# Kernel tuning notes

Hardware: AMD Instinct MI355X
Metric: run time of the kernel (lower is better)

Reference implementation:

```python
import jax, jax.numpy as jnp
import numpy as np

N_NODES = 100_000
N_EDGES = 3_200_000
NUM_FEATURES = 128
EMB = 128
GNN_LAYERS = 3
N_GRAPHS = 512
FILL = 2.0  # improved=True -> self-loop weight 2


def setup_inputs() -> dict:
    key = jax.random.key(0)
    ks = jax.random.split(key, 8)
    x = jax.random.normal(ks[0], (N_NODES, NUM_FEATURES), jnp.float32)
    edge_index = jax.random.randint(ks[1], (2, N_EDGES), 0, N_NODES, dtype=jnp.int64)
    batch_index = jnp.sort(jax.random.randint(ks[2], (N_NODES,), 0, N_GRAPHS, dtype=jnp.int64))
    W0 = jax.random.normal(ks[3], (NUM_FEATURES, EMB), jnp.float32) / np.float32(np.sqrt(NUM_FEATURES))
    b0 = jnp.zeros((EMB,), jnp.float32)
    W_hid = jax.random.normal(ks[4], (GNN_LAYERS - 1, EMB, EMB), jnp.float32) / np.float32(np.sqrt(EMB))
    b_hid = jnp.zeros((GNN_LAYERS - 1, EMB), jnp.float32)
    W_out = jax.random.normal(ks[5], (2 * EMB, 1), jnp.float32) / np.float32(np.sqrt(2 * EMB))
    b_out = jnp.zeros((1,), jnp.float32)
    return {"x": x, "edge_index": edge_index, "batch_index": batch_index,
            "W0": W0, "b0": b0, "W_hid": W_hid, "b_hid": b_hid,
            "W_out": W_out, "b_out": b_out}


def _gcn_norm(edge_index, n_nodes):
    # add self-loops (weight=FILL for improved=True), symmetric D^-1/2 A D^-1/2 norm
    loop = jnp.arange(n_nodes)
    row = jnp.concatenate([edge_index[0], loop])
    col = jnp.concatenate([edge_index[1], loop])
    w = jnp.concatenate([jnp.ones((edge_index.shape[1],), jnp.float32),
                         jnp.full((n_nodes,), FILL, jnp.float32)])
    deg = jax.ops.segment_sum(w, col, num_segments=n_nodes)
    dinv = jnp.where(deg > 0, jax.lax.rsqrt(deg), 0.0)
    return row, col, dinv[row] * w * dinv[col]


def _gcn_conv(h, W, b, row, col, norm, n_nodes):
    h = h @ W                              # [N, emb]
    msg = h[row] * norm[:, None]           # gather + scale over edges
    return jax.ops.segment_sum(msg, col, num_segments=n_nodes) + b


def reference(x, edge_index, batch_index, W0, b0, W_hid, b_hid, W_out, b_out):
    n = x.shape[0]
    row, col, norm = _gcn_norm(edge_index, n)
    h = jnp.tanh(_gcn_conv(x, W0, b0, row, col, norm, n))
    for i in range(W_hid.shape[0]):
        h = jnp.tanh(_gcn_conv(h, W_hid[i], b_hid[i], row, col, norm, n))
    cnt = jax.ops.segment_sum(jnp.ones((n,), h.dtype), batch_index, num_segments=N_GRAPHS)
    mx = jax.ops.segment_max(h, batch_index, num_segments=N_GRAPHS)
    mx = jnp.where(cnt[:, None] > 0, mx, 0.0)            # gmp
    mean = jax.ops.segment_sum(h, batch_index, num_segments=N_GRAPHS) / jnp.maximum(cnt, 1.0)[:, None]  # gap
    pooled = jnp.concatenate([mx, mean], axis=1)          # [G, 2*emb]
    return pooled @ W_out + b_out                         # [G, 1]
```

## Files before the change

### kernel.cpp

```cpp
#include <hip/hip_runtime.h>
#include <math.h>

#define NF 128
#define SCAN_CHUNK 1024
#define BUCK_SHIFT 9
#define BUCK_CAP 20480
#define NBUCK_MAX 256
#define ECHUNK 2048

typedef int      vint4   __attribute__((ext_vector_type(4)));
typedef float    vfloat4 __attribute__((ext_vector_type(4)));
typedef float    f32x4   __attribute__((ext_vector_type(4)));
typedef _Float16 vhalf4  __attribute__((ext_vector_type(4)));
typedef _Float16 vhalf8  __attribute__((ext_vector_type(8)));

__global__ __launch_bounds__(256) void k_bucket(const int* __restrict__ row,
                                                const int* __restrict__ col,
                                                int* __restrict__ gcur,
                                                int* __restrict__ bdata, int E) {
  __shared__ int bcnt[NBUCK_MAX];
  __shared__ int bstage[NBUCK_MAX][32];
  const int tid = threadIdx.x;
  const int nChunks = (E + ECHUNK - 1) / ECHUNK;

  for (int chunk = blockIdx.x; chunk < nChunks; chunk += gridDim.x) {
    bcnt[tid] = 0;
    __syncthreads();

    const int cbase = chunk * ECHUNK;
    if (cbase + ECHUNK <= E) {
      const vint4* r4 = reinterpret_cast<const vint4*>(row) + (cbase >> 2) + 2 * tid;
      const vint4* c4 = reinterpret_cast<const vint4*>(col) + (cbase >> 2) + 2 * tid;
      vint4 ra = __builtin_nontemporal_load(&r4[0]);
      vint4 rb = __builtin_nontemporal_load(&r4[1]);
      vint4 ca = __builtin_nontemporal_load(&c4[0]);
      vint4 cb = __builtin_nontemporal_load(&c4[1]);
      int rr[8] = {ra.x, ra.y, ra.z, ra.w, rb.x, rb.y, rb.z, rb.w};
      int cc[8] = {ca.x, ca.y, ca.z, ca.w, cb.x, cb.y, cb.z, cb.w};
#pragma unroll
      for (int j = 0; j < 8; ++j) {
        int b = cc[j] >> BUCK_SHIFT;
        int packed = ((cc[j] & ((1 << BUCK_SHIFT) - 1)) << 17) | rr[j];
        int pos = atomicAdd(&bcnt[b], 1);
        if (pos < 32) {
          bstage[b][pos] = packed;
        } else {
          int p = atomicAdd(&gcur[b], 1);
          if (p < BUCK_CAP) bdata[b * BUCK_CAP + p] = packed;
        }
      }
    } else {
      for (int j = 0; j < 8; ++j) {
        int e = cbase + tid + j * 256;
        if (e < E) {
          int c = col[e], r = row[e];
          int b = c >> BUCK_SHIFT;
          int packed = ((c & ((1 << BUCK_SHIFT) - 1)) << 17) | r;
          int pos = atomicAdd(&bcnt[b], 1);
          if (pos < 32) {
            bstage[b][pos] = packed;
          } else {
            int p = atomicAdd(&gcur[b], 1);
            if (p < BUCK_CAP) bdata[b * BUCK_CAP + p] = packed;
          }
        }
      }
    }
    __syncthreads();

    int k = bcnt[tid];
    if (k > 32) k = 32;
    if (k > 0) {
      int p = atomicAdd(&gcur[tid], k);
      for (int i = 0; i < k && p + i < BUCK_CAP; ++i)
        bdata[tid * BUCK_CAP + p + i] = bstage[tid][i];
    }
    __syncthreads();
  }
}

__global__ __launch_bounds__(256) void k_hist(const int* __restrict__ gcur,
                                              const int* __restrict__ bdata,
                                              int* __restrict__ cnt, int N) {
  __shared__ int hist[1 << BUCK_SHIFT];
  const int b = blockIdx.x;
  const int tid = threadIdx.x;
  hist[tid] = 0;
  hist[tid + 256] = 0;
  __syncthreads();
  int nb = gcur[b];
  if (nb > BUCK_CAP) nb = BUCK_CAP;
  const int* bd = bdata + (size_t)b * BUCK_CAP;
  for (int i = tid; i < nb; i += 256) atomicAdd(&hist[bd[i] >> 17], 1);
  __syncthreads();
  int base = b << BUCK_SHIFT;
#pragma unroll
  for (int k = 0; k < (1 << BUCK_SHIFT); k += 256) {
    int node = base + k + tid;
    if (node < N) cnt[node] = hist[k + tid];
  }
}

__global__ __launch_bounds__(256) void k_scanA(const int* __restrict__ cnt,
                                               int* __restrict__ chunkTot, int N) {
  int c0 = blockIdx.x * SCAN_CHUNK + threadIdx.x * 4;
  int s = 0;
#pragma unroll
  for (int j = 0; j < 4; ++j) {
    int idx = c0 + j;
    if (idx < N) s += cnt[idx];
  }
  __shared__ int red[256];
  red[threadIdx.x] = s;
  __syncthreads();
  for (int o = 128; o > 0; o >>= 1) {
    if (threadIdx.x < o) red[threadIdx.x] += red[threadIdx.x + o];
    __syncthreads();
  }
  if (threadIdx.x == 0) chunkTot[blockIdx.x] = red[0];
}

__global__ __launch_bounds__(128) void k_scanB(const int* __restrict__ chunkTot,
                                               int* __restrict__ chunkOff, int nChunks) {
  __shared__ int buf[128];
  int t = threadIdx.x;
  int v = (t < nChunks) ? chunkTot[t] : 0;
  buf[t] = v;
  __syncthreads();
  for (int o = 1; o < 128; o <<= 1) {
    int x = buf[t];
    if (t >= o) x += buf[t - o];
    __syncthreads();
    buf[t] = x;
    __syncthreads();
  }
  if (t < nChunks) chunkOff[t] = buf[t] - v;
}

__global__ __launch_bounds__(256) void k_scanC(const int* __restrict__ cnt,
                                               const int* __restrict__ chunkOff,
                                               int* __restrict__ offs,
                                               float* __restrict__ dinv, int N) {
  int t = threadIdx.x;
  int c0 = blockIdx.x * SCAN_CHUNK + t * 4;
  int v[4];
  int s = 0;
#pragma unroll
  for (int j = 0; j < 4; ++j) {
    int idx = c0 + j;
    v[j] = (idx < N) ? cnt[idx] : 0;
    s += v[j];
  }
  __shared__ int buf[256];
  buf[t] = s;
  __syncthreads();
  for (int o = 1; o < 256; o <<= 1) {
    int x = buf[t];
    if (t >= o) x += buf[t - o];
    __syncthreads();
    buf[t] = x;
    __syncthreads();
  }
  int excl = buf[t] - s + chunkOff[blockIdx.x];
#pragma unroll
  for (int j = 0; j < 4; ++j) {
    int idx = c0 + j;
    if (idx < N) {
      offs[idx] = excl;
      dinv[idx] = rsqrtf((float)v[j] + 2.0f);
      excl += v[j];
    }
  }
}

__global__ __launch_bounds__(256) void k_bfill(const int* __restrict__ gcur,
                                               const int* __restrict__ bdata,
                                               const int* __restrict__ offs,
                                               int* __restrict__ csr, int N) {
  __shared__ int lcur[1 << BUCK_SHIFT];
  const int b = blockIdx.x;
  const int tid = threadIdx.x;
  const int base = b << BUCK_SHIFT;
#pragma unroll
  for (int k = 0; k < (1 << BUCK_SHIFT); k += 256) {
    int node = base + k + tid;
    lcur[k + tid] = (node < N) ? offs[node] : 0;
  }
  __syncthreads();
  int nb = gcur[b];
  if (nb > BUCK_CAP) nb = BUCK_CAP;
  const int* bd = bdata + (size_t)b * BUCK_CAP;
  for (int i = tid; i < nb; i += 256) {
    int v = bd[i];
    int p = atomicAdd(&lcur[v >> 17], 1);
    csr[p] = v & 0x1FFFF;
  }
}

__global__ __launch_bounds__(256) void k_wcvt(const float* __restrict__ W0,
                                              const float* __restrict__ Whid,
                                              _Float16* __restrict__ wt) {
  int g = blockIdx.x * 1024 + threadIdx.x * 4;
#pragma unroll
  for (int j = 0; j < 4; ++j) {
    int idx = g + j;
    int layer = idx >> 14;
    int within = idx & 16383;
    int c = within >> 7, k = within & 127;
    const float* src = (layer == 0) ? W0 : Whid + (layer - 1) * 16384;
    wt[idx] = (_Float16)src[k * 128 + c];
  }
}

template <bool F32IN>
__global__ __launch_bounds__(256) void k_gemm(const void* __restrict__ Hin,
                                              const _Float16* __restrict__ Wt,
                                              const float* __restrict__ dinv,
                                              _Float16* __restrict__ out, int nRows) {
  __shared__ _Float16 Wl[128][136];

  const int tid = threadIdx.x;
  for (int i = tid; i < 128 * 16; i += 256) {
    int r = i >> 4, seg = i & 15;
    *reinterpret_cast<vhalf8*>(&Wl[r][seg * 8]) =
        *reinterpret_cast<const vhalf8*>(Wt + r * 128 + seg * 8);
  }
  __syncthreads();

  const int l = tid & 63;
  const int wv = tid >> 6;
  const int lrow = l & 15;
  const int lk8 = (l >> 4) * 8;
  const int nTiles = (nRows + 63) / 64;

#pragma unroll 1
  for (int tile = blockIdx.x; tile < nTiles; tile += gridDim.x) {
    const int rowBase = tile * 64 + wv * 16;

    vhalf8 a[4];
    int arow = rowBase + lrow;
    if (arow < nRows) {
      if constexpr (F32IN) {
        const float* ap = (const float*)Hin + (size_t)arow * 128 + lk8;
#pragma unroll
        for (int kc = 0; kc < 4; ++kc) {
          vfloat4 lo = *reinterpret_cast<const vfloat4*>(ap + kc * 32);
          vfloat4 hi = *reinterpret_cast<const vfloat4*>(ap + kc * 32 + 4);
          vhalf8 v;
          v[0] = (_Float16)lo.x; v[1] = (_Float16)lo.y;
          v[2] = (_Float16)lo.z; v[3] = (_Float16)lo.w;
          v[4] = (_Float16)hi.x; v[5] = (_Float16)hi.y;
          v[6] = (_Float16)hi.z; v[7] = (_Float16)hi.w;
          a[kc] = v;
        }
      } else {
        const _Float16* ap = (const _Float16*)Hin + (size_t)arow * 128 + lk8;
#pragma unroll
        for (int kc = 0; kc < 4; ++kc)
          a[kc] = *reinterpret_cast<const vhalf8*>(ap + kc * 32);
      }
    } else {
#pragma unroll
      for (int kc = 0; kc < 4; ++kc)
#pragma unroll
        for (int j = 0; j < 8; ++j) a[kc][j] = (_Float16)0.f;
    }

    f32x4 acc[8];
#pragma unroll
    for (int ct = 0; ct < 8; ++ct) acc[ct] = (f32x4)(0.f);

#pragma unroll
    for (int kc = 0; kc < 4; ++kc) {
#pragma unroll
      for (int ct = 0; ct < 8; ++ct) {
        vhalf8 b = *reinterpret_cast<const vhalf8*>(&Wl[ct * 16 + lrow][kc * 32 + lk8]);
        acc[ct] = __builtin_amdgcn_mfma_f32_16x16x32_f16(a[kc], b, acc[ct], 0, 0, 0);
      }
    }

    const int r0 = rowBase + (l >> 4) * 4;
    float dv[4];
#pragma unroll
    for (int r = 0; r < 4; ++r) dv[r] = (r0 + r < nRows) ? dinv[r0 + r] : 0.f;
#pragma unroll
    for (int ct = 0; ct < 8; ++ct) {
#pragma unroll
      for (int r = 0; r < 4; ++r) {
        int row = r0 + r;
        if (row < nRows)
          out[(size_t)row * 128 + ct * 16 + lrow] = (_Float16)(dv[r] * acc[ct][r]);
      }
    }
  }
}

__device__ __forceinline__ float4 h2f(vhalf4 v) {
  return make_float4((float)v.x, (float)v.y, (float)v.z, (float)v.w);
}
__device__ __forceinline__ float4 add4(float4 a, float4 acc) {
  acc.x += a.x; acc.y += a.y; acc.z += a.z; acc.w += a.w;
  return acc;
}

__global__ __launch_bounds__(256) void k_agg(const _Float16* __restrict__ tmp,
                                             const int* __restrict__ offs,
                                             const int* __restrict__ cnt,
                                             const int* __restrict__ csr,
                                             const float* __restrict__ dinv,
                                             const float* __restrict__ bias,
                                             _Float16* __restrict__ hout, int N) {
  int node = (blockIdx.x * 256 + threadIdx.x) >> 5;
  if (node >= N) return;
  int lane = threadIdx.x & 31;

  float dv = dinv[node];

  const vhalf4* t4 = reinterpret_cast<const vhalf4*>(tmp);
  float4 hv = h2f(t4[(size_t)node * 32 + lane]);
  float4 acc = make_float4(2.f * hv.x, 2.f * hv.y, 2.f * hv.z, 2.f * hv.w);

  int s = offs[node], e = s + cnt[node];
  int i = s;

  for (; (i & 3) && i < e; ++i) {
    float4 a = h2f(t4[(size_t)csr[i] * 32 + lane]);
    acc = add4(a, acc);
  }

  const vint4* cp = reinterpret_cast<const vint4*>(csr);
  for (; i + 8 <= e; i += 8) {
    vint4 p0 = __builtin_nontemporal_load(&cp[(i >> 2) + 0]);
    vint4 p1 = __builtin_nontemporal_load(&cp[(i >> 2) + 1]);
    float4 a0 = h2f(t4[(size_t)p0.x * 32 + lane]);
    float4 a1 = h2f(t4[(size_t)p0.y * 32 + lane]);
    float4 a2 = h2f(t4[(size_t)p0.z * 32 + lane]);
    float4 a3 = h2f(t4[(size_t)p0.w * 32 + lane]);
    float4 a4 = h2f(t4[(size_t)p1.x * 32 + lane]);
    float4 a5 = h2f(t4[(size_t)p1.y * 32 + lane]);
    float4 a6 = h2f(t4[(size_t)p1.z * 32 + lane]);
    float4 a7 = h2f(t4[(size_t)p1.w * 32 + lane]);
    acc = add4(a0, acc); acc = add4(a1, acc);
    acc = add4(a2, acc); acc = add4(a3, acc);
    acc = add4(a4, acc); acc = add4(a5, acc);
    acc = add4(a6, acc); acc = add4(a7, acc);
  }
  for (; i + 4 <= e; i += 4) {
    vint4 p = __builtin_nontemporal_load(&cp[i >> 2]);
    float4 a0 = h2f(t4[(size_t)p.x * 32 + lane]);
    float4 a1 = h2f(t4[(size_t)p.y * 32 + lane]);
    float4 a2 = h2f(t4[(size_t)p.z * 32 + lane]);
    float4 a3 = h2f(t4[(size_t)p.w * 32 + lane]);
    acc = add4(a0, acc); acc = add4(a1, acc);
    acc = add4(a2, acc); acc = add4(a3, acc);
  }
  for (; i < e; ++i) {
    float4 a = h2f(t4[(size_t)csr[i] * 32 + lane]);
    acc = add4(a, acc);
  }

  float4 b4 = reinterpret_cast<const float4*>(bias)[lane];
  vhalf4 r;
  r.x = (_Float16)tanhf(fmaf(dv, acc.x, b4.x));
  r.y = (_Float16)tanhf(fmaf(dv, acc.y, b4.y));
  r.z = (_Float16)tanhf(fmaf(dv, acc.z, b4.z));
  r.w = (_Float16)tanhf(fmaf(dv, acc.w, b4.w));
  __builtin_nontemporal_store(r, &reinterpret_cast<vhalf4*>(hout)[(size_t)node * 32 + lane]);
}

__global__ __launch_bounds__(512) void k_pool(const _Float16* __restrict__ h,
                                              const int* __restrict__ batch,
                                              const float* __restrict__ Wout,
                                              const float* __restrict__ bout,
                                              float* __restrict__ out, int N) {
  int g = blockIdx.x;

  int lo = 0, hi = N;
  while (lo < hi) { int mid = (lo + hi) >> 1; if (batch[mid] < g) lo = mid + 1; else hi = mid; }
  int s = lo;
  int lo2 = s, hi2 = N;
  while (lo2 < hi2) { int mid = (lo2 + hi2) >> 1; if (batch[mid] < g + 1) lo2 = mid + 1; else hi2 = mid; }
  int e = lo2;

  int f = threadIdx.x & 127;
  int stripe = threadIdx.x >> 7;

  float mx = -INFINITY, sm = 0.f;
  for (int n = s + stripe; n < e; n += 4) {
    float v = (float)h[(size_t)n * NF + f];
    mx = fmaxf(mx, v);
    sm += v;
  }

  __shared__ float smx[4][NF];
  __shared__ float ssm[4][NF];
  smx[stripe][f] = mx;
  ssm[stripe][f] = sm;
  __syncthreads();

  if (stripe == 0) {
    mx = fmaxf(fmaxf(smx[0][f], smx[1][f]), fmaxf(smx[2][f], smx[3][f]));
    sm = ssm[0][f] + ssm[1][f] + ssm[2][f] + ssm[3][f];

    int cnt = e - s;
    float mean = sm / fmaxf((float)cnt, 1.0f);
    if (cnt == 0) mx = 0.f;

    float part = mx * Wout[f] + mean * Wout[NF + f];

    for (int o = 32; o > 0; o >>= 1) part += __shfl_down(part, o);
    __shared__ float wsum[2];
    if ((threadIdx.x & 63) == 0) wsum[threadIdx.x >> 6] = part;
    __syncthreads();
    if (threadIdx.x == 0) out[g] = wsum[0] + wsum[1] + bout[0];
  }
}

extern "C" void kernel_launch(void* const* d_in, const int* in_sizes, int n_in,
                              void* d_out, int out_size, void* d_ws, size_t ws_size,
                              hipStream_t stream) {
  const float* x     = (const float*)d_in[0];
  const int*   eidx  = (const int*)d_in[1];
  const int*   batch = (const int*)d_in[2];
  const float* W0    = (const float*)d_in[3];
  const float* b0    = (const float*)d_in[4];
  const float* Whid  = (const float*)d_in[5];
  const float* bhid  = (const float*)d_in[6];
  const float* Wout  = (const float*)d_in[7];
  const float* bout  = (const float*)d_in[8];
  float* out = (float*)d_out;

  const int N = in_sizes[0] / NF;
  const int E = in_sizes[1] / 2;
  const int G = out_size;

  const int* erow = eidx;
  const int* ecol = eidx + E;

  size_t off = 0;
  auto alloc = [&](size_t bytes) -> void* {
    void* p = (char*)d_ws + off;
    off += (bytes + 255) & ~(size_t)255;
    return p;
  };
  int*      gcur     = (int*)alloc(NBUCK_MAX * 4);
  int*      cnt      = (int*)alloc((size_t)N * 4);
  float*    dinv     = (float*)alloc((size_t)N * 4);
  int*      offs     = (int*)alloc((size_t)N * 4);
  int*      chunkTot = (int*)alloc(1024);
  int*      chunkOff = (int*)alloc(1024);
  int*      bdata    = (int*)alloc((size_t)NBUCK_MAX * BUCK_CAP * 4);
  int*      csr      = (int*)alloc((size_t)E * 4);
  _Float16* wt       = (_Float16*)alloc(3 * 16384 * 2);
  _Float16* tmp      = (_Float16*)alloc((size_t)N * NF * 2);
  _Float16* h        = (_Float16*)alloc((size_t)N * NF * 2);
  (void)ws_size;

  (void)hipMemsetAsync(gcur, 0, NBUCK_MAX * 4, stream);

  const int nChunks = (N + SCAN_CHUNK - 1) / SCAN_CHUNK;
  const int nbuck = (N + (1 << BUCK_SHIFT) - 1) >> BUCK_SHIFT;

  k_bucket<<<512, 256, 0, stream>>>(erow, ecol, gcur, bdata, E);
  k_hist<<<nbuck, 256, 0, stream>>>(gcur, bdata, cnt, N);
  k_scanA<<<nChunks, 256, 0, stream>>>(cnt, chunkTot, N);
  k_scanB<<<1, 128, 0, stream>>>(chunkTot, chunkOff, nChunks);
  k_scanC<<<nChunks, 256, 0, stream>>>(cnt, chunkOff, offs, dinv, N);
  k_bfill<<<nbuck, 256, 0, stream>>>(gcur, bdata, offs, csr, N);
  k_wcvt<<<48, 256, 0, stream>>>(W0, Whid, wt);

  const int nTiles = (N + 63) / 64;
  const int gemmGrid = (nTiles < 784) ? nTiles : 784;
  const int aggGrid = (N + 7) / 8;

  k_gemm<true><<<gemmGrid, 256, 0, stream>>>(x, wt, dinv, tmp, N);
  k_agg<<<aggGrid, 256, 0, stream>>>(tmp, offs, cnt, csr, dinv, b0, h, N);
  k_gemm<false><<<gemmGrid, 256, 0, stream>>>(h, wt + 16384, dinv, tmp, N);
  k_agg<<<aggGrid, 256, 0, stream>>>(tmp, offs, cnt, csr, dinv, bhid, h, N);
  k_gemm<false><<<gemmGrid, 256, 0, stream>>>(h, wt + 2 * 16384, dinv, tmp, N);
  k_agg<<<aggGrid, 256, 0, stream>>>(tmp, offs, cnt, csr, dinv, bhid + NF, h, N);

  k_pool<<<G, 512, 0, stream>>>(h, batch, Wout, bout, out, N);
}
```

Baseline: 567.3 us.

## Transpose GEMM MFMA operands for vectorized stores, drop LDS weight staging

The GEMM kernel swaps the MFMA operand order so each lane's accumulator holds four consecutive output features of one node. This lets every lane write a packed 4-half vector instead of scattered 2-byte stores. The shared-memory weight staging and the persistent grid-stride loop are removed: weights are read directly from global memory (cache-resident), and one 64-row tile is launched per block. The trade-off is that every block re-reads the 32KB weight matrix through cache instead of loading it once into LDS per block.

```diff
diff --git a/kernel.cpp b/kernel.cpp
--- a/kernel.cpp
+++ b/kernel.cpp
@@ -217,80 +217,66 @@
                                               const _Float16* __restrict__ Wt,
                                               const float* __restrict__ dinv,
                                               _Float16* __restrict__ out, int nRows) {
-  __shared__ _Float16 Wl[128][136];
-
   const int tid = threadIdx.x;
-  for (int i = tid; i < 128 * 16; i += 256) {
-    int r = i >> 4, seg = i & 15;
-    *reinterpret_cast<vhalf8*>(&Wl[r][seg * 8]) =
-        *reinterpret_cast<const vhalf8*>(Wt + r * 128 + seg * 8);
-  }
-  __syncthreads();
-
   const int l = tid & 63;
   const int wv = tid >> 6;
-  const int lrow = l & 15;
+  const int lidx = l & 15;
   const int lk8 = (l >> 4) * 8;
-  const int nTiles = (nRows + 63) / 64;
-
-#pragma unroll 1
-  for (int tile = blockIdx.x; tile < nTiles; tile += gridDim.x) {
-    const int rowBase = tile * 64 + wv * 16;
-
-    vhalf8 a[4];
-    int arow = rowBase + lrow;
-    if (arow < nRows) {
-      if constexpr (F32IN) {
-        const float* ap = (const float*)Hin + (size_t)arow * 128 + lk8;
-#pragma unroll
-        for (int kc = 0; kc < 4; ++kc) {
-          vfloat4 lo = *reinterpret_cast<const vfloat4*>(ap + kc * 32);
-          vfloat4 hi = *reinterpret_cast<const vfloat4*>(ap + kc * 32 + 4);
-          vhalf8 v;
-          v[0] = (_Float16)lo.x; v[1] = (_Float16)lo.y;
-          v[2] = (_Float16)lo.z; v[3] = (_Float16)lo.w;
-          v[4] = (_Float16)hi.x; v[5] = (_Float16)hi.y;
-          v[6] = (_Float16)hi.z; v[7] = (_Float16)hi.w;
-          a[kc] = v;
-        }
-      } else {
-        const _Float16* ap = (const _Float16*)Hin + (size_t)arow * 128 + lk8;
-#pragma unroll
-        for (int kc = 0; kc < 4; ++kc)
-          a[kc] = *reinterpret_cast<const vhalf8*>(ap + kc * 32);
+  const int node = blockIdx.x * 64 + wv * 16 + lidx;
+
+  vhalf8 hfrag[4];
+  if (node < nRows) {
+    if constexpr (F32IN) {
+      const float* hp = (const float*)Hin + (size_t)node * NF + lk8;
+#pragma unroll
+      for (int kc = 0; kc < 4; ++kc) {
+        vfloat4 lo = *reinterpret_cast<const vfloat4*>(hp + kc * 32);
+        vfloat4 hi = *reinterpret_cast<const vfloat4*>(hp + kc * 32 + 4);
+        vhalf8 v;
+        v[0] = (_Float16)lo.x; v[1] = (_Float16)lo.y;
+        v[2] = (_Float16)lo.z; v[3] = (_Float16)lo.w;
+        v[4] = (_Float16)hi.x; v[5] = (_Float16)hi.y;
+        v[6] = (_Float16)hi.z; v[7] = (_Float16)hi.w;
+        hfrag[kc] = v;
       }
     } else {
+      const _Float16* hp = (const _Float16*)Hin + (size_t)node * NF + lk8;
 #pragma unroll
       for (int kc = 0; kc < 4; ++kc)
-#pragma unroll
-        for (int j = 0; j < 8; ++j) a[kc][j] = (_Float16)0.f;
-    }
-
-    f32x4 acc[8];
-#pragma unroll
-    for (int ct = 0; ct < 8; ++ct) acc[ct] = (f32x4)(0.f);
-
-#pragma unroll
-    for (int kc = 0; kc < 4; ++kc) {
-#pragma unroll
-      for (int ct = 0; ct < 8; ++ct) {
-        vhalf8 b = *reinterpret_cast<const vhalf8*>(&Wl[ct * 16 + lrow][kc * 32 + lk8]);
-        acc[ct] = __builtin_amdgcn_mfma_f32_16x16x32_f16(a[kc], b, acc[ct], 0, 0, 0);
-      }
-    }
-
-    const int r0 = rowBase + (l >> 4) * 4;
-    float dv[4];
-#pragma unroll
-    for (int r = 0; r < 4; ++r) dv[r] = (r0 + r < nRows) ? dinv[r0 + r] : 0.f;
+        hfrag[kc] = *reinterpret_cast<const vhalf8*>(hp + kc * 32);
+    }
+  } else {
+#pragma unroll
+    for (int kc = 0; kc < 4; ++kc)
+#pragma unroll
+      for (int j = 0; j < 8; ++j) hfrag[kc][j] = (_Float16)0.f;
+  }
+
+  f32x4 acc[8];
+#pragma unroll
+  for (int ct = 0; ct < 8; ++ct) acc[ct] = (f32x4)(0.f);
+
+  const _Float16* wp = Wt + (size_t)lidx * NF + lk8;
+#pragma unroll
+  for (int kc = 0; kc < 4; ++kc) {
 #pragma unroll
     for (int ct = 0; ct < 8; ++ct) {
-#pragma unroll
-      for (int r = 0; r < 4; ++r) {
-        int row = r0 + r;
-        if (row < nRows)
-          out[(size_t)row * 128 + ct * 16 + lrow] = (_Float16)(dv[r] * acc[ct][r]);
-      }
+      vhalf8 w = *reinterpret_cast<const vhalf8*>(wp + ct * 16 * NF + kc * 32);
+      acc[ct] = __builtin_amdgcn_mfma_f32_16x16x32_f16(w, hfrag[kc], acc[ct], 0, 0, 0);
+    }
+  }
+
+  if (node < nRows) {
+    float dv = dinv[node];
+    const int f0 = (l >> 4) * 4;
+#pragma unroll
+    for (int ct = 0; ct < 8; ++ct) {
+      vhalf4 o;
+      o.x = (_Float16)(dv * acc[ct][0]);
+      o.y = (_Float16)(dv * acc[ct][1]);
+      o.z = (_Float16)(dv * acc[ct][2]);
+      o.w = (_Float16)(dv * acc[ct][3]);
+      *reinterpret_cast<vhalf4*>(out + (size_t)node * NF + ct * 16 + f0) = o;
     }
   }
 }
@@ -469,8 +455,7 @@
   k_bfill<<<nbuck, 256, 0, stream>>>(gcur, bdata, offs, csr, N);
   k_wcvt<<<48, 256, 0, stream>>>(W0, Whid, wt);
 
-  const int nTiles = (N + 63) / 64;
-  const int gemmGrid = (nTiles < 784) ? nTiles : 784;
+  const int gemmGrid = (N + 63) / 64;
   const int aggGrid = (N + 7) / 8;
 
   k_gemm<true><<<gemmGrid, 256, 0, stream>>>(x, wt, dinv, tmp, N);
```

Result: slower. 588.8 us (+3.8%).
